# Kernel tuning notes

Hardware: AMD Instinct MI355X
Metric: run time of the kernel (lower is better)

Reference implementation:

```python
import jax, jax.numpy as jnp
import numpy as np

B, NQ, D, H, P, BEV, FFN = 8, 900, 256, 8, 4, 200, 512
HD = D // H
RADIUS = 0.2


def _ln(x, s, b):
    m = x.mean(-1, keepdims=True)
    v = ((x - m) ** 2).mean(-1, keepdims=True)
    return (x - m) / jnp.sqrt(v + 1e-5) * s + b


def _grid_sample(feat, grid):
    # feat: [BH, C, Hh, Ww]; grid: [BH, Q, P, 2] in [-1, 1]
    # bilinear, padding_mode='zeros', align_corners=False (matches F.grid_sample)
    BH, C, Hh, Ww = feat.shape
    gx = (grid[..., 0] + 1.0) * (Ww * 0.5) - 0.5
    gy = (grid[..., 1] + 1.0) * (Hh * 0.5) - 0.5
    x0 = jnp.floor(gx)
    y0 = jnp.floor(gy)
    wx1 = gx - x0
    wy1 = gy - y0

    def corner(xi, yi, w):
        valid = (xi >= 0) & (xi < Ww) & (yi >= 0) & (yi < Hh)
        xc = jnp.clip(xi, 0, Ww - 1).astype(jnp.int32)
        yc = jnp.clip(yi, 0, Hh - 1).astype(jnp.int32)
        vals = jax.vmap(lambda fm, yy, xx: fm[:, yy, xx])(feat, yc, xc)  # [BH, C, Q, P]
        return vals * (w * valid)[:, None, :, :]

    return (corner(x0, y0, (1 - wx1) * (1 - wy1))
            + corner(x0 + 1, y0, wx1 * (1 - wy1))
            + corner(x0, y0 + 1, (1 - wx1) * wy1)
            + corner(x0 + 1, y0 + 1, wx1 * wy1))


def _forward(query, memory, reference_points, query_pos,
             in_w, in_b, out_w, out_b,
             off_w, off_b, wt_w, wt_b, co_w, co_b,
             f_w1, f_b1, f_w2, f_b2,
             n1s, n1b, n2s, n2b, n3s, n3b, bev_h, bev_w):
    b, nq, d = query.shape
    # ---- self-attention (eval mode: dropout = identity) ----
    q_in = _ln(query + query_pos, n1s, n1b)
    qkv = q_in @ in_w.T + in_b
    q, k, v = jnp.split(qkv, 3, axis=-1)
    q = q.reshape(b, nq, H, HD)
    k = k.reshape(b, nq, H, HD)
    v = v.reshape(b, nq, H, HD)
    scores = jnp.einsum('bqhd,bkhd->bhqk', q, k) * (1.0 / HD ** 0.5)
    attn = jax.nn.softmax(scores, axis=-1)
    self_out = jnp.einsum('bhqk,bkhd->bqhd', attn, v).reshape(b, nq, d) @ out_w.T + out_b
    query = query + self_out
    # ---- deformable cross-attention over BEV memory ----
    q2 = _ln(query + query_pos, n2s, n2b)
    offsets = jnp.tanh(q2 @ off_w.T + off_b).reshape(b, nq, H, P, 2) * RADIUS
    weights = jax.nn.softmax((q2 @ wt_w.T + wt_b).reshape(b, nq, H, P), axis=-1)
    locations = reference_points[:, :, None, None, :2] + offsets  # [b, nq, H, P, 2]
    feat = memory.transpose(0, 2, 1).reshape(b * H, HD, bev_h, bev_w)
    grid = locations.transpose(0, 2, 1, 3, 4).reshape(b * H, nq, P, 2) * 2.0 - 1.0
    sampled = _grid_sample(feat, grid).reshape(b, H, HD, nq, P)
    fused = jnp.einsum('bhdqp,bqhp->bqhd', sampled, weights).reshape(b, nq, d)
    query = query + (fused @ co_w.T + co_b)
    # ---- FFN ----
    q3 = _ln(query, n3s, n3b)
    ffn = jax.nn.relu(q3 @ f_w1.T + f_b1) @ f_w2.T + f_b2
    return query + ffn


def setup_inputs() -> dict:
    key = jax.random.key(0)
    ks = jax.random.split(key, 16)
    s = 0.02
    return dict(
        query=jax.random.normal(ks[0], (B, NQ, D), jnp.float32),
        memory=jax.random.normal(ks[1], (B, BEV * BEV, D), jnp.float32),
        reference_points=jax.random.uniform(ks[2], (B, NQ, 2), jnp.float32),
        query_pos=jax.random.normal(ks[3], (B, NQ, D), jnp.float32),
        in_w=jax.random.normal(ks[4], (3 * D, D), jnp.float32) * s,
        in_b=jnp.zeros((3 * D,), jnp.float32),
        out_w=jax.random.normal(ks[5], (D, D), jnp.float32) * s,
        out_b=jnp.zeros((D,), jnp.float32),
        off_w=jax.random.normal(ks[6], (H * P * 2, D), jnp.float32) * s,
        off_b=jnp.zeros((H * P * 2,), jnp.float32),
        wt_w=jax.random.normal(ks[7], (H * P, D), jnp.float32) * s,
        wt_b=jnp.zeros((H * P,), jnp.float32),
        co_w=jax.random.normal(ks[8], (D, D), jnp.float32) * s,
        co_b=jnp.zeros((D,), jnp.float32),
        f_w1=jax.random.normal(ks[9], (FFN, D), jnp.float32) * s,
        f_b1=jnp.zeros((FFN,), jnp.float32),
        f_w2=jax.random.normal(ks[10], (D, FFN), jnp.float32) * s,
        f_b2=jnp.zeros((D,), jnp.float32),
        n1s=jnp.ones((D,), jnp.float32), n1b=jnp.zeros((D,), jnp.float32),
        n2s=jnp.ones((D,), jnp.float32), n2b=jnp.zeros((D,), jnp.float32),
        n3s=jnp.ones((D,), jnp.float32), n3b=jnp.zeros((D,), jnp.float32),
        bev_h=BEV, bev_w=BEV,
    )


def reference(query, memory, reference_points, query_pos,
              in_w, in_b, out_w, out_b,
              off_w, off_b, wt_w, wt_b, co_w, co_b,
              f_w1, f_b1, f_w2, f_b2,
              n1s, n1b, n2s, n2b, n3s, n3b, bev_h, bev_w):
    return _forward(query, memory, reference_points, query_pos,
                    in_w, in_b, out_w, out_b,
                    off_w, off_b, wt_w, wt_b, co_w, co_b,
                    f_w1, f_b1, f_w2, f_b2,
                    n1s, n1b, n2s, n2b, n3s, n3b, bev_h, bev_w)
```

## Files before the change

kernel.cpp:

```cpp
#include <hip/hip_runtime.h>
#include <math.h>

#define B_   8
#define NQ_  900
#define D_   256
#define H_   8
#define P_   4
#define BEV_ 200
#define FFN_ 512
#define HD_  32
#define M_   (B_*NQ_)
#define NKPAD 960

typedef __attribute__((ext_vector_type(8))) short short8;
typedef __attribute__((ext_vector_type(4))) float floatx4;

__device__ inline unsigned short f2bf(float f) {
    union { float f; unsigned u; } v; v.f = f;
    unsigned r = v.u + 0x7fffu + ((v.u >> 16) & 1u);
    return (unsigned short)(r >> 16);
}
__device__ inline float bf2f(unsigned short h) {
    union { unsigned u; float f; } v; v.u = ((unsigned)h) << 16;
    return v.f;
}

__global__ __launch_bounds__(256)
void convert_weights(const float* __restrict__ in_w, const float* __restrict__ out_w,
                     const float* __restrict__ off_w, const float* __restrict__ wt_w,
                     const float* __restrict__ co_w, const float* __restrict__ f_w1,
                     const float* __restrict__ f_w2, const float* __restrict__ off_b,
                     const float* __restrict__ wt_b,
                     unsigned short* __restrict__ wb, float* __restrict__ bias_ow)
{
    int i = blockIdx.x * 256 + threadIdx.x;
    if (i < 196608)      { wb[i] = f2bf(in_w[i]); }
    else if (i < 262144) { wb[i] = f2bf(out_w[i - 196608]); }
    else if (i < 278528) { wb[i] = f2bf(off_w[i - 262144]); }
    else if (i < 286720) { wb[i] = f2bf(wt_w[i - 278528]); }
    else if (i < 352256) { wb[i] = f2bf(co_w[i - 286720]); }
    else if (i < 483328) { wb[i] = f2bf(f_w1[i - 352256]); }
    else if (i < 614400) { wb[i] = f2bf(f_w2[i - 483328]); }
    else if (i < 614464) { bias_ow[i - 614400] = off_b[i - 614400]; }
    else if (i < 614496) { bias_ow[i - 614400] = wt_b[i - 614464]; }
}

__global__ __launch_bounds__(256)
void ln_kernel(const float* __restrict__ x, const float* __restrict__ pos,
               const float* __restrict__ gamma, const float* __restrict__ beta,
               unsigned short* __restrict__ out, int rows)
{
    int w    = threadIdx.x >> 6;
    int lane = threadIdx.x & 63;
    int row  = blockIdx.x * 4 + w;
    if (row >= rows) return;
    size_t base = (size_t)row * D_ + lane * 4;
    float4 v = *(const float4*)(x + base);
    if (pos) {
        float4 p = *(const float4*)(pos + base);
        v.x += p.x; v.y += p.y; v.z += p.z; v.w += p.w;
    }
    float s = v.x + v.y + v.z + v.w;
    float q = v.x*v.x + v.y*v.y + v.z*v.z + v.w*v.w;
    #pragma unroll
    for (int o = 1; o < 64; o <<= 1) {
        s += __shfl_xor(s, o, 64);
        q += __shfl_xor(q, o, 64);
    }
    float m   = s * (1.0f / D_);
    float var = q * (1.0f / D_) - m * m;
    float inv = rsqrtf(var + 1e-5f);
    float4 g = *(const float4*)(gamma + lane * 4);
    float4 b = *(const float4*)(beta  + lane * 4);
    ushort4 o4;
    o4.x = f2bf((v.x - m) * inv * g.x + b.x);
    o4.y = f2bf((v.y - m) * inv * g.y + b.y);
    o4.z = f2bf((v.z - m) * inv * g.z + b.z);
    o4.w = f2bf((v.w - m) * inv * g.w + b.w);
    *(ushort4*)(out + base) = o4;
}

template<int RELU, int OUTBF>
__global__ __launch_bounds__(256)
void gemm_mfma(const unsigned short* __restrict__ A, const unsigned short* __restrict__ W,
               const float* __restrict__ bias, const float* __restrict__ res,
               float* __restrict__ outf, unsigned short* __restrict__ outb,
               int M, int N, int K)
{
    __shared__ unsigned short As[128 * 32];
    __shared__ unsigned short Bs[128 * 32];
    const int t    = threadIdx.x;
    const int m0   = blockIdx.y * 128;
    const int n0   = blockIdx.x * 128;
    const int lane = t & 63;
    const int w    = t >> 6;
    const int wm   = (w >> 1) * 64;
    const int wn   = (w & 1) * 64;
    const int lr   = lane & 15;
    const int kq   = lane >> 4;

    floatx4 acc[4][4];
    #pragma unroll
    for (int i = 0; i < 4; ++i)
        #pragma unroll
        for (int j = 0; j < 4; ++j) acc[i][j] = (floatx4){0.f, 0.f, 0.f, 0.f};

    const int sr = t >> 1;
    const int sc = (t & 1) * 2;

    for (int k0 = 0; k0 < K; k0 += 32) {
        uint4 a0 = {0,0,0,0}, a1 = {0,0,0,0};
        int gm = m0 + sr;
        if (gm < M) {
            const uint4* src = (const uint4*)(A + (size_t)gm * K + k0 + sc * 8);
            a0 = src[0]; a1 = src[1];
        }
        *(uint4*)&As[sr * 32 + ((sc    ) ^ (sr & 3)) * 8] = a0;
        *(uint4*)&As[sr * 32 + ((sc + 1) ^ (sr & 3)) * 8] = a1;
        uint4 b0 = {0,0,0,0}, b1 = {0,0,0,0};
        int gn = n0 + sr;
        if (gn < N) {
            const uint4* src = (const uint4*)(W + (size_t)gn * K + k0 + sc * 8);
            b0 = src[0]; b1 = src[1];
        }
        *(uint4*)&Bs[sr * 32 + ((sc    ) ^ (sr & 3)) * 8] = b0;
        *(uint4*)&Bs[sr * 32 + ((sc + 1) ^ (sr & 3)) * 8] = b1;
        __syncthreads();

        short8 af[4], bfr[4];
        #pragma unroll
        for (int i = 0; i < 4; ++i) {
            int ra = wm + i * 16 + lr;
            af[i] = *(const short8*)&As[ra * 32 + (kq ^ (ra & 3)) * 8];
            int rb = wn + i * 16 + lr;
            bfr[i] = *(const short8*)&Bs[rb * 32 + (kq ^ (rb & 3)) * 8];
        }
        #pragma unroll
        for (int mi = 0; mi < 4; ++mi)
            #pragma unroll
            for (int ni = 0; ni < 4; ++ni)
                acc[mi][ni] = __builtin_amdgcn_mfma_f32_16x16x32_bf16(
                    af[mi], bfr[ni], acc[mi][ni], 0, 0, 0);
        __syncthreads();
    }

    const int rbase = kq * 4;
    #pragma unroll
    for (int ni = 0; ni < 4; ++ni) {
        int n = n0 + wn + ni * 16 + lr;
        if (n >= N) continue;
        float bv = bias[n];
        #pragma unroll
        for (int mi = 0; mi < 4; ++mi) {
            floatx4 c = acc[mi][ni];
            #pragma unroll
            for (int r = 0; r < 4; ++r) {
                int m = m0 + wm + mi * 16 + rbase + r;
                if (m < M) {
                    float vl = c[r] + bv;
                    if (res) vl += res[(size_t)m * N + n];
                    if (RELU) vl = fmaxf(vl, 0.f);
                    if (OUTBF) outb[(size_t)m * N + n] = f2bf(vl);
                    else       outf[(size_t)m * N + n] = vl;
                }
            }
        }
    }
}

__global__ __launch_bounds__(256)
void repack_qkv(const unsigned short* __restrict__ qkv,
                unsigned short* __restrict__ Qb, unsigned short* __restrict__ Kb,
                unsigned short* __restrict__ Vt)
{
    int tid = blockIdx.x * 256 + threadIdx.x;
    if (tid >= 64 * NKPAD * 32) return;
    int ch  = tid & 31;
    int key = (tid >> 5) % NKPAD;
    int bh  = tid / (NKPAD * 32);
    int b = bh >> 3, h = bh & 7;
    unsigned short qv = 0, kv = 0, vv = 0;
    if (key < NQ_) {
        const unsigned short* row = qkv + ((size_t)(b * NQ_ + key)) * 768 + h * 32 + ch;
        qv = f2bf(bf2f(row[0]) * 0.17677669529663687f);
        kv = row[256];
        vv = row[512];
    }
    size_t qk_idx = (size_t)bh * NKPAD * 32 + key * 32 + ch;
    Qb[qk_idx] = qv;
    Kb[qk_idx] = kv;
    Vt[(size_t)(bh * 32 + ch) * NKPAD + key] = vv;
}

__global__ __launch_bounds__(256)
void flash_attn(const unsigned short* __restrict__ Qb, const unsigned short* __restrict__ Kb,
                const unsigned short* __restrict__ Vt, unsigned short* __restrict__ out)
{
    __shared__ unsigned short P_lds[4][16][72];
    const int bh   = blockIdx.y;
    const int b    = bh >> 3, h = bh & 7;
    const int q0   = blockIdx.x * 64;
    const int w    = threadIdx.x >> 6;
    const int lane = threadIdx.x & 63;
    const int lr   = lane & 15;
    const int quad = lane >> 4;

    const short8 qfrag = *(const short8*)(Qb + ((size_t)bh * NKPAD + q0 + w * 16 + lr) * 32 + quad * 8);

    floatx4 O0 = (floatx4){0.f,0.f,0.f,0.f};
    floatx4 O1 = (floatx4){0.f,0.f,0.f,0.f};
    float m_i[4] = {-INFINITY, -INFINITY, -INFINITY, -INFINITY};
    float l_i[4] = {0.f, 0.f, 0.f, 0.f};

    const unsigned short* kbase_p = Kb + (size_t)bh * NKPAD * 32;
    const unsigned short* vbase_p = Vt + (size_t)bh * 32 * NKPAD;

    for (int kt = 0; kt < 15; ++kt) {
        const int kb = kt * 64;
        short8 kf[4];
        #pragma unroll
        for (int ni = 0; ni < 4; ++ni)
            kf[ni] = *(const short8*)(kbase_p + (size_t)(kb + ni * 16 + lr) * 32 + quad * 8);
        floatx4 S[4];
        #pragma unroll
        for (int ni = 0; ni < 4; ++ni)
            S[ni] = __builtin_amdgcn_mfma_f32_16x16x32_bf16(
                qfrag, kf[ni], (floatx4){0.f,0.f,0.f,0.f}, 0, 0, 0);
        if (kt == 14) {
            #pragma unroll
            for (int ni = 0; ni < 4; ++ni) {
                int key = kb + ni * 16 + lr;
                if (key >= NQ_) S[ni] = (floatx4){-1e30f, -1e30f, -1e30f, -1e30f};
            }
        }
        float rowmax[4];
        #pragma unroll
        for (int r = 0; r < 4; ++r)
            rowmax[r] = fmaxf(fmaxf(S[0][r], S[1][r]), fmaxf(S[2][r], S[3][r]));
        #pragma unroll
        for (int off = 1; off < 16; off <<= 1)
            #pragma unroll
            for (int r = 0; r < 4; ++r)
                rowmax[r] = fmaxf(rowmax[r], __shfl_xor(rowmax[r], off, 64));
        float alpha[4], rs[4];
        #pragma unroll
        for (int r = 0; r < 4; ++r) {
            float mnew = fmaxf(m_i[r], rowmax[r]);
            alpha[r] = __expf(m_i[r] - mnew);
            m_i[r] = mnew;
            rs[r] = 0.f;
        }
        #pragma unroll
        for (int ni = 0; ni < 4; ++ni) {
            #pragma unroll
            for (int r = 0; r < 4; ++r) {
                float p = __expf(S[ni][r] - m_i[r]);
                rs[r] += p;
                P_lds[w][quad * 4 + r][ni * 16 + lr] = f2bf(p);
            }
        }
        #pragma unroll
        for (int off = 1; off < 16; off <<= 1)
            #pragma unroll
            for (int r = 0; r < 4; ++r)
                rs[r] += __shfl_xor(rs[r], off, 64);
        #pragma unroll
        for (int r = 0; r < 4; ++r) {
            l_i[r] = alpha[r] * l_i[r] + rs[r];
            O0[r] *= alpha[r];
            O1[r] *= alpha[r];
        }
        asm volatile("s_waitcnt lgkmcnt(0)" ::: "memory");
        short8 pf0 = *(const short8*)&P_lds[w][lr][quad * 8];
        short8 pf1 = *(const short8*)&P_lds[w][lr][32 + quad * 8];
        short8 vf;
        vf = *(const short8*)(vbase_p + (size_t)(lr) * NKPAD + kb + quad * 8);
        O0 = __builtin_amdgcn_mfma_f32_16x16x32_bf16(pf0, vf, O0, 0, 0, 0);
        vf = *(const short8*)(vbase_p + (size_t)(lr) * NKPAD + kb + 32 + quad * 8);
        O0 = __builtin_amdgcn_mfma_f32_16x16x32_bf16(pf1, vf, O0, 0, 0, 0);
        vf = *(const short8*)(vbase_p + (size_t)(16 + lr) * NKPAD + kb + quad * 8);
        O1 = __builtin_amdgcn_mfma_f32_16x16x32_bf16(pf0, vf, O1, 0, 0, 0);
        vf = *(const short8*)(vbase_p + (size_t)(16 + lr) * NKPAD + kb + 32 + quad * 8);
        O1 = __builtin_amdgcn_mfma_f32_16x16x32_bf16(pf1, vf, O1, 0, 0, 0);
        asm volatile("s_waitcnt lgkmcnt(0)" ::: "memory");
    }
    #pragma unroll
    for (int r = 0; r < 4; ++r) {
        int q = q0 + w * 16 + quad * 4 + r;
        if (q < NQ_) {
            float inv = 1.f / l_i[r];
            size_t base = ((size_t)(b * NQ_ + q)) * D_ + h * 32;
            out[base + lr]      = f2bf(O0[r] * inv);
            out[base + 16 + lr] = f2bf(O1[r] * inv);
        }
    }
}

__global__ __launch_bounds__(256)
void prep_kernel(const float* __restrict__ offwt, const float* __restrict__ refp,
                 float4* __restrict__ sx, float4* __restrict__ sy, float4* __restrict__ sw)
{
    int idx = blockIdx.x * 256 + threadIdx.x;
    if (idx >= B_ * NQ_ * H_) return;
    int h  = idx & 7;
    int bq = idx >> 3;
    const float* orow = offwt + (size_t)bq * 96 + h * 8;
    const float* wrow = offwt + (size_t)bq * 96 + 64 + h * 4;
    float rx = refp[bq * 2 + 0];
    float ry = refp[bq * 2 + 1];
    float gx[4], gy[4], wv[4];
    #pragma unroll
    for (int p = 0; p < 4; ++p) {
        float ox = tanhf(orow[p * 2 + 0]) * 0.2f;
        float oy = tanhf(orow[p * 2 + 1]) * 0.2f;
        gx[p] = (rx + ox) * (float)BEV_ - 0.5f;
        gy[p] = (ry + oy) * (float)BEV_ - 0.5f;
        wv[p] = wrow[p];
    }
    float mx = fmaxf(fmaxf(wv[0], wv[1]), fmaxf(wv[2], wv[3]));
    float e0 = expf(wv[0]-mx), e1 = expf(wv[1]-mx), e2 = expf(wv[2]-mx), e3 = expf(wv[3]-mx);
    float inv = 1.f / (e0 + e1 + e2 + e3);
    sx[idx] = make_float4(gx[0], gx[1], gx[2], gx[3]);
    sy[idx] = make_float4(gy[0], gy[1], gy[2], gy[3]);
    sw[idx] = make_float4(e0*inv, e1*inv, e2*inv, e3*inv);
}

__global__ __launch_bounds__(256)
void sample_kernel(const float* __restrict__ mem,
                   const float4* __restrict__ sx, const float4* __restrict__ sy,
                   const float4* __restrict__ sw, unsigned short* __restrict__ fused)
{
    int tid = blockIdx.x * 256 + threadIdx.x;
    if (tid >= B_ * NQ_ * H_ * HD_) return;
    int d   = tid & 31;
    int bqh = tid >> 5;
    int h   = bqh & 7;
    int bq  = bqh >> 3;
    int b   = bq / NQ_;
    const float* mb = mem + (size_t)b * (BEV_ * BEV_) * D_ + h * HD_ + d;
    float4 X = sx[bqh], Y = sy[bqh], W = sw[bqh];
    float xs[4] = {X.x, X.y, X.z, X.w};
    float ys[4] = {Y.x, Y.y, Y.z, Y.w};
    float ws[4] = {W.x, W.y, W.z, W.w};
    float acc = 0.f;
    #pragma unroll
    for (int p = 0; p < 4; ++p) {
        float gx = xs[p], gy = ys[p];
        float x0f = floorf(gx), y0f = floorf(gy);
        int x0 = (int)x0f, y0 = (int)y0f;
        float wx1 = gx - x0f, wy1 = gy - y0f;
        float wx0 = 1.f - wx1, wy0 = 1.f - wy1;
        float s = 0.f;
        #pragma unroll
        for (int cy = 0; cy < 2; ++cy) {
            int yy = y0 + cy;
            if (yy < 0 || yy >= BEV_) continue;
            float wyv = cy ? wy1 : wy0;
            #pragma unroll
            for (int cx = 0; cx < 2; ++cx) {
                int xx = x0 + cx;
                if (xx < 0 || xx >= BEV_) continue;
                float wxv = cx ? wx1 : wx0;
                s += wyv * wxv * mb[((size_t)yy * BEV_ + xx) * D_];
            }
        }
        acc += ws[p] * s;
    }
    fused[(size_t)bq * D_ + h * HD_ + d] = f2bf(acc);
}

extern "C" void kernel_launch(void* const* d_in, const int* in_sizes, int n_in,
                              void* d_out, int out_size, void* d_ws, size_t ws_size,
                              hipStream_t stream) {
    const float* query     = (const float*)d_in[0];
    const float* memory    = (const float*)d_in[1];
    const float* refp      = (const float*)d_in[2];
    const float* query_pos = (const float*)d_in[3];
    const float* in_w  = (const float*)d_in[4];
    const float* in_b  = (const float*)d_in[5];
    const float* out_w = (const float*)d_in[6];
    const float* out_b = (const float*)d_in[7];
    const float* off_w = (const float*)d_in[8];
    const float* off_b = (const float*)d_in[9];
    const float* wt_w  = (const float*)d_in[10];
    const float* wt_b  = (const float*)d_in[11];
    const float* co_w  = (const float*)d_in[12];
    const float* co_b  = (const float*)d_in[13];
    const float* f_w1  = (const float*)d_in[14];
    const float* f_b1  = (const float*)d_in[15];
    const float* f_w2  = (const float*)d_in[16];
    const float* f_b2  = (const float*)d_in[17];
    const float* n1s = (const float*)d_in[18];
    const float* n1b = (const float*)d_in[19];
    const float* n2s = (const float*)d_in[20];
    const float* n2b = (const float*)d_in[21];
    const float* n3s = (const float*)d_in[22];
    const float* n3b = (const float*)d_in[23];
    float* outp = (float*)d_out;

    char* w = (char*)d_ws;
    unsigned short* wb      = (unsigned short*)w;
    float*          bias_ow = (float*)(w + 1228800);
    unsigned short* ln_bf   = (unsigned short*)(w + 1229184);
    float*          q1      = (float*)(w + 4915584);
    unsigned short* qkv_bf  = (unsigned short*)(w + 12288384);
    unsigned short* Qb      = (unsigned short*)(w + 23347584);
    unsigned short* Kb      = (unsigned short*)(w + 27279744);
    unsigned short* Vt      = (unsigned short*)(w + 31211904);
    float*          offwt   = (float*)(w + 12288384);
    float*          samp    = (float*)(w + 15053184);
    unsigned short* fuse_bf = (unsigned short*)(w + 17817984);
    unsigned short* h1_bf   = (unsigned short*)(w + 12288384);
    unsigned short* attn_bf = ln_bf;

    const unsigned short* wb_in  = wb;
    const unsigned short* wb_out = wb + 196608;
    const unsigned short* wb_ow  = wb + 262144;
    const unsigned short* wb_co  = wb + 286720;
    const unsigned short* wb_f1  = wb + 352256;
    const unsigned short* wb_f2  = wb + 483328;

    dim3 blk(256);
    const int M = M_;

    convert_weights<<<dim3((614496 + 255) / 256), blk, 0, stream>>>(
        in_w, out_w, off_w, wt_w, co_w, f_w1, f_w2, off_b, wt_b, wb, bias_ow);
    ln_kernel<<<dim3(M / 4), blk, 0, stream>>>(query, query_pos, n1s, n1b, ln_bf, M);
    gemm_mfma<0,1><<<dim3(6, 57), blk, 0, stream>>>(ln_bf, wb_in, in_b, nullptr,
                                                    nullptr, qkv_bf, M, 768, 256);
    repack_qkv<<<dim3(64 * NKPAD * 32 / 256), blk, 0, stream>>>(qkv_bf, Qb, Kb, Vt);
    flash_attn<<<dim3(15, 64), blk, 0, stream>>>(Qb, Kb, Vt, attn_bf);
    gemm_mfma<0,0><<<dim3(2, 57), blk, 0, stream>>>(attn_bf, wb_out, out_b, query,
                                                    q1, nullptr, M, 256, 256);
    ln_kernel<<<dim3(M / 4), blk, 0, stream>>>(q1, query_pos, n2s, n2b, ln_bf, M);
    gemm_mfma<0,0><<<dim3(1, 57), blk, 0, stream>>>(ln_bf, wb_ow, bias_ow, nullptr,
                                                    offwt, nullptr, M, 96, 256);
    prep_kernel<<<dim3((B_ * NQ_ * H_ + 255) / 256), blk, 0, stream>>>(
        offwt, refp, (float4*)samp, (float4*)samp + 57600, (float4*)samp + 115200);
    sample_kernel<<<dim3(B_ * NQ_ * H_ * HD_ / 256), blk, 0, stream>>>(
        memory, (const float4*)samp, (const float4*)samp + 57600,
        (const float4*)samp + 115200, fuse_bf);
    gemm_mfma<0,0><<<dim3(2, 57), blk, 0, stream>>>(fuse_bf, wb_co, co_b, q1,
                                                    outp, nullptr, M, 256, 256);
    ln_kernel<<<dim3(M / 4), blk, 0, stream>>>(outp, nullptr, n3s, n3b, ln_bf, M);
    gemm_mfma<1,1><<<dim3(4, 57), blk, 0, stream>>>(ln_bf, wb_f1, f_b1, nullptr,
                                                    nullptr, h1_bf, M, 512, 256);
    gemm_mfma<0,0><<<dim3(2, 57), blk, 0, stream>>>(h1_bf, wb_f2, f_b2, outp,
                                                    outp, nullptr, M, 256, 512);
}
```

Before: 680.6 us.

## Fuse QKV repack into GEMM epilogue, merge prologue kernels, fuse offset prep

The QKV projection GEMM now writes scaled Q, K and transposed V straight into the padded attention layouts, which removes the separate repack kernel and the intermediate qkv buffer. Weight conversion, zeroing of the padding rows and the first LayerNorm are merged into one prologue launch. The offset/weight GEMM stages its tile in LDS and computes the tanh offsets and softmax weights in its epilogue, replacing the prep kernel. Together these cut kernel launches and global round trips. The cost is scattered 2-byte stores in the QKV epilogue, plus extra LDS use in the fused offset GEMM.

```diff
diff --git a/kernel.cpp b/kernel.cpp
--- a/kernel.cpp
+++ b/kernel.cpp
@@ -26,23 +26,74 @@
 }
 
 __global__ __launch_bounds__(256)
-void convert_weights(const float* __restrict__ in_w, const float* __restrict__ out_w,
-                     const float* __restrict__ off_w, const float* __restrict__ wt_w,
-                     const float* __restrict__ co_w, const float* __restrict__ f_w1,
-                     const float* __restrict__ f_w2, const float* __restrict__ off_b,
-                     const float* __restrict__ wt_b,
-                     unsigned short* __restrict__ wb, float* __restrict__ bias_ow)
+void prologue(const float* __restrict__ in_w, const float* __restrict__ out_w,
+              const float* __restrict__ off_w, const float* __restrict__ wt_w,
+              const float* __restrict__ co_w, const float* __restrict__ f_w1,
+              const float* __restrict__ f_w2, const float* __restrict__ off_b,
+              const float* __restrict__ wt_b,
+              unsigned short* __restrict__ wb, float* __restrict__ bias_ow,
+              unsigned short* __restrict__ Qb, unsigned short* __restrict__ Kb,
+              unsigned short* __restrict__ Vt,
+              const float* __restrict__ query, const float* __restrict__ query_pos,
+              const float* __restrict__ n1s, const float* __restrict__ n1b,
+              unsigned short* __restrict__ ln_out)
 {
-    int i = blockIdx.x * 256 + threadIdx.x;
-    if (i < 196608)      { wb[i] = f2bf(in_w[i]); }
-    else if (i < 262144) { wb[i] = f2bf(out_w[i - 196608]); }
-    else if (i < 278528) { wb[i] = f2bf(off_w[i - 262144]); }
-    else if (i < 286720) { wb[i] = f2bf(wt_w[i - 278528]); }
-    else if (i < 352256) { wb[i] = f2bf(co_w[i - 286720]); }
-    else if (i < 483328) { wb[i] = f2bf(f_w1[i - 352256]); }
-    else if (i < 614400) { wb[i] = f2bf(f_w2[i - 483328]); }
-    else if (i < 614464) { bias_ow[i - 614400] = off_b[i - 614400]; }
-    else if (i < 614496) { bias_ow[i - 614400] = wt_b[i - 614464]; }
+    const int bx = blockIdx.x;
+    const int t  = threadIdx.x;
+    if (bx < 2401) {
+        int i = bx * 256 + t;
+        if (i < 196608)      { wb[i] = f2bf(in_w[i]); }
+        else if (i < 262144) { wb[i] = f2bf(out_w[i - 196608]); }
+        else if (i < 278528) { wb[i] = f2bf(off_w[i - 262144]); }
+        else if (i < 286720) { wb[i] = f2bf(wt_w[i - 278528]); }
+        else if (i < 352256) { wb[i] = f2bf(co_w[i - 286720]); }
+        else if (i < 483328) { wb[i] = f2bf(f_w1[i - 352256]); }
+        else if (i < 614400) { wb[i] = f2bf(f_w2[i - 483328]); }
+        else if (i < 614464) { bias_ow[i - 614400] = off_b[i - 614400]; }
+        else if (i < 614496) { bias_ow[i - 614400] = wt_b[i - 614464]; }
+    } else if (bx < 2881) {
+        int j  = (bx - 2401) * 256 + t;
+        int bh = j / 1920;
+        int rem = j - bh * 1920;
+        int q  = 900 + (rem >> 5);
+        int ch = rem & 31;
+        size_t idx = ((size_t)bh * NKPAD + q) * 32 + ch;
+        Qb[idx] = 0;
+        Kb[idx] = 0;
+    } else if (bx < 3361) {
+        int j  = (bx - 2881) * 256 + t;
+        int bh = j / 1920;
+        int rem = j - bh * 1920;
+        int ch = rem / 60;
+        int k  = rem - ch * 60;
+        Vt[((size_t)bh * 32 + ch) * NKPAD + 900 + k] = 0;
+    } else {
+        int w    = t >> 6;
+        int lane = t & 63;
+        int row  = (bx - 3361) * 4 + w;
+        size_t base = (size_t)row * D_ + lane * 4;
+        float4 v = *(const float4*)(query + base);
+        float4 p = *(const float4*)(query_pos + base);
+        v.x += p.x; v.y += p.y; v.z += p.z; v.w += p.w;
+        float s = v.x + v.y + v.z + v.w;
+        float q = v.x*v.x + v.y*v.y + v.z*v.z + v.w*v.w;
+        #pragma unroll
+        for (int o = 1; o < 64; o <<= 1) {
+            s += __shfl_xor(s, o, 64);
+            q += __shfl_xor(q, o, 64);
+        }
+        float m   = s * (1.0f / D_);
+        float var = q * (1.0f / D_) - m * m;
+        float inv = rsqrtf(var + 1e-5f);
+        float4 g = *(const float4*)(n1s + lane * 4);
+        float4 b = *(const float4*)(n1b + lane * 4);
+        ushort4 o4;
+        o4.x = f2bf((v.x - m) * inv * g.x + b.x);
+        o4.y = f2bf((v.y - m) * inv * g.y + b.y);
+        o4.z = f2bf((v.z - m) * inv * g.z + b.z);
+        o4.w = f2bf((v.w - m) * inv * g.w + b.w);
+        *(ushort4*)(ln_out + base) = o4;
+    }
 }
 
 __global__ __launch_bounds__(256)
@@ -80,11 +131,13 @@
     *(ushort4*)(out + base) = o4;
 }
 
-template<int RELU, int OUTBF>
+template<int RELU, int OUTBF, int QKVOUT>
 __global__ __launch_bounds__(256)
 void gemm_mfma(const unsigned short* __restrict__ A, const unsigned short* __restrict__ W,
                const float* __restrict__ bias, const float* __restrict__ res,
                float* __restrict__ outf, unsigned short* __restrict__ outb,
+               unsigned short* __restrict__ Qb, unsigned short* __restrict__ Kb,
+               unsigned short* __restrict__ Vt,
                int M, int N, int K)
 {
     __shared__ unsigned short As[128 * 32];
@@ -150,46 +203,157 @@
         int n = n0 + wn + ni * 16 + lr;
         if (n >= N) continue;
         float bv = bias[n];
+        if (QKVOUT) {
+            const int type = n >> 8;
+            const int hh   = (n >> 5) & 7;
+            const int ch   = n & 31;
+            #pragma unroll
+            for (int mi = 0; mi < 4; ++mi) {
+                floatx4 c = acc[mi][ni];
+                #pragma unroll
+                for (int r = 0; r < 4; ++r) {
+                    int m = m0 + wm + mi * 16 + rbase + r;
+                    if (m < M) {
+                        float vl = c[r] + bv;
+                        int bb = m / 900;
+                        int qq = m - bb * 900;
+                        size_t bh = (size_t)(bb * 8 + hh);
+                        if (type == 0)
+                            Qb[(bh * NKPAD + qq) * 32 + ch] = f2bf(vl * 0.17677669529663687f);
+                        else if (type == 1)
+                            Kb[(bh * NKPAD + qq) * 32 + ch] = f2bf(vl);
+                        else
+                            Vt[(bh * 32 + ch) * NKPAD + qq] = f2bf(vl);
+                    }
+                }
+            }
+        } else {
+            #pragma unroll
+            for (int mi = 0; mi < 4; ++mi) {
+                floatx4 c = acc[mi][ni];
+                #pragma unroll
+                for (int r = 0; r < 4; ++r) {
+                    int m = m0 + wm + mi * 16 + rbase + r;
+                    if (m < M) {
+                        float vl = c[r] + bv;
+                        if (res) vl += res[(size_t)m * N + n];
+                        if (RELU) vl = fmaxf(vl, 0.f);
+                        if (OUTBF) outb[(size_t)m * N + n] = f2bf(vl);
+                        else       outf[(size_t)m * N + n] = vl;
+                    }
+                }
+            }
+        }
+    }
+}
+
+__global__ __launch_bounds__(256)
+void gemm_offwt_prep(const unsigned short* __restrict__ A, const unsigned short* __restrict__ W,
+                     const float* __restrict__ bias, const float* __restrict__ refp,
+                     float4* __restrict__ sx, float4* __restrict__ sy, float4* __restrict__ sw)
+{
+    __shared__ unsigned short As[128 * 32];
+    __shared__ unsigned short Bs[128 * 32];
+    __shared__ float T[128][100];
+    const int t    = threadIdx.x;
+    const int m0   = blockIdx.y * 128;
+    const int lane = t & 63;
+    const int w    = t >> 6;
+    const int wm   = (w >> 1) * 64;
+    const int wn   = (w & 1) * 64;
+    const int lr   = lane & 15;
+    const int kq   = lane >> 4;
+    const int M = M_, N = 96, K = 256;
+
+    floatx4 acc[4][4];
+    #pragma unroll
+    for (int i = 0; i < 4; ++i)
+        #pragma unroll
+        for (int j = 0; j < 4; ++j) acc[i][j] = (floatx4){0.f, 0.f, 0.f, 0.f};
+
+    const int sr = t >> 1;
+    const int sc = (t & 1) * 2;
+
+    for (int k0 = 0; k0 < K; k0 += 32) {
+        uint4 a0 = {0,0,0,0}, a1 = {0,0,0,0};
+        int gm = m0 + sr;
+        if (gm < M) {
+            const uint4* src = (const uint4*)(A + (size_t)gm * K + k0 + sc * 8);
+            a0 = src[0]; a1 = src[1];
+        }
+        *(uint4*)&As[sr * 32 + ((sc    ) ^ (sr & 3)) * 8] = a0;
+        *(uint4*)&As[sr * 32 + ((sc + 1) ^ (sr & 3)) * 8] = a1;
+        uint4 b0 = {0,0,0,0}, b1 = {0,0,0,0};
+        int gn = sr;
+        if (gn < N) {
+            const uint4* src = (const uint4*)(W + (size_t)gn * K + k0 + sc * 8);
+            b0 = src[0]; b1 = src[1];
+        }
+        *(uint4*)&Bs[sr * 32 + ((sc    ) ^ (sr & 3)) * 8] = b0;
+        *(uint4*)&Bs[sr * 32 + ((sc + 1) ^ (sr & 3)) * 8] = b1;
+        __syncthreads();
+
+        short8 af[4], bfr[4];
+        #pragma unroll
+        for (int i = 0; i < 4; ++i) {
+            int ra = wm + i * 16 + lr;
+            af[i] = *(const short8*)&As[ra * 32 + (kq ^ (ra & 3)) * 8];
+            int rb = wn + i * 16 + lr;
+            bfr[i] = *(const short8*)&Bs[rb * 32 + (kq ^ (rb & 3)) * 8];
+        }
+        #pragma unroll
+        for (int mi = 0; mi < 4; ++mi)
+            #pragma unroll
+            for (int ni = 0; ni < 4; ++ni)
+                acc[mi][ni] = __builtin_amdgcn_mfma_f32_16x16x32_bf16(
+                    af[mi], bfr[ni], acc[mi][ni], 0, 0, 0);
+        __syncthreads();
+    }
+
+    const int rbase = kq * 4;
+    #pragma unroll
+    for (int ni = 0; ni < 4; ++ni) {
+        int n = wn + ni * 16 + lr;
+        if (n >= N) continue;
+        float bv = bias[n];
         #pragma unroll
         for (int mi = 0; mi < 4; ++mi) {
             floatx4 c = acc[mi][ni];
             #pragma unroll
-            for (int r = 0; r < 4; ++r) {
-                int m = m0 + wm + mi * 16 + rbase + r;
-                if (m < M) {
-                    float vl = c[r] + bv;
-                    if (res) vl += res[(size_t)m * N + n];
-                    if (RELU) vl = fmaxf(vl, 0.f);
-                    if (OUTBF) outb[(size_t)m * N + n] = f2bf(vl);
-                    else       outf[(size_t)m * N + n] = vl;
-                }
-            }
-        }
-    }
-}
-
-__global__ __launch_bounds__(256)
-void repack_qkv(const unsigned short* __restrict__ qkv,
-                unsigned short* __restrict__ Qb, unsigned short* __restrict__ Kb,
-                unsigned short* __restrict__ Vt)
-{
-    int tid = blockIdx.x * 256 + threadIdx.x;
-    if (tid >= 64 * NKPAD * 32) return;
-    int ch  = tid & 31;
-    int key = (tid >> 5) % NKPAD;
-    int bh  = tid / (NKPAD * 32);
-    int b = bh >> 3, h = bh & 7;
-    unsigned short qv = 0, kv = 0, vv = 0;
-    if (key < NQ_) {
-        const unsigned short* row = qkv + ((size_t)(b * NQ_ + key)) * 768 + h * 32 + ch;
-        qv = f2bf(bf2f(row[0]) * 0.17677669529663687f);
-        kv = row[256];
-        vv = row[512];
-    }
-    size_t qk_idx = (size_t)bh * NKPAD * 32 + key * 32 + ch;
-    Qb[qk_idx] = qv;
-    Kb[qk_idx] = kv;
-    Vt[(size_t)(bh * 32 + ch) * NKPAD + key] = vv;
+            for (int r = 0; r < 4; ++r)
+                T[wm + mi * 16 + rbase + r][n] = c[r] + bv;
+        }
+    }
+    __syncthreads();
+
+    #pragma unroll
+    for (int it = 0; it < 4; ++it) {
+        int item = t + it * 256;
+        int row  = item >> 3;
+        int h    = item & 7;
+        int gq   = m0 + row;
+        if (gq >= M) continue;
+        float rx = refp[gq * 2 + 0];
+        float ry = refp[gq * 2 + 1];
+        const float* orow = &T[row][h * 8];
+        const float* wrow = &T[row][64 + h * 4];
+        float gx[4], gy[4], wv[4];
+        #pragma unroll
+        for (int p = 0; p < 4; ++p) {
+            float ox = tanhf(orow[p * 2 + 0]) * 0.2f;
+            float oy = tanhf(orow[p * 2 + 1]) * 0.2f;
+            gx[p] = (rx + ox) * (float)BEV_ - 0.5f;
+            gy[p] = (ry + oy) * (float)BEV_ - 0.5f;
+            wv[p] = wrow[p];
+        }
+        float mx = fmaxf(fmaxf(wv[0], wv[1]), fmaxf(wv[2], wv[3]));
+        float e0 = expf(wv[0]-mx), e1 = expf(wv[1]-mx), e2 = expf(wv[2]-mx), e3 = expf(wv[3]-mx);
+        float inv = 1.f / (e0 + e1 + e2 + e3);
+        int idx = gq * 8 + h;
+        sx[idx] = make_float4(gx[0], gx[1], gx[2], gx[3]);
+        sy[idx] = make_float4(gy[0], gy[1], gy[2], gy[3]);
+        sw[idx] = make_float4(e0*inv, e1*inv, e2*inv, e3*inv);
+    }
 }
 
 __global__ __launch_bounds__(256)
@@ -294,35 +458,6 @@
             out[base + 16 + lr] = f2bf(O1[r] * inv);
         }
     }
-}
-
-__global__ __launch_bounds__(256)
-void prep_kernel(const float* __restrict__ offwt, const float* __restrict__ refp,
-                 float4* __restrict__ sx, float4* __restrict__ sy, float4* __restrict__ sw)
-{
-    int idx = blockIdx.x * 256 + threadIdx.x;
-    if (idx >= B_ * NQ_ * H_) return;
-    int h  = idx & 7;
-    int bq = idx >> 3;
-    const float* orow = offwt + (size_t)bq * 96 + h * 8;
-    const float* wrow = offwt + (size_t)bq * 96 + 64 + h * 4;
-    float rx = refp[bq * 2 + 0];
-    float ry = refp[bq * 2 + 1];
-    float gx[4], gy[4], wv[4];
-    #pragma unroll
-    for (int p = 0; p < 4; ++p) {
-        float ox = tanhf(orow[p * 2 + 0]) * 0.2f;
-        float oy = tanhf(orow[p * 2 + 1]) * 0.2f;
-        gx[p] = (rx + ox) * (float)BEV_ - 0.5f;
-        gy[p] = (ry + oy) * (float)BEV_ - 0.5f;
-        wv[p] = wrow[p];
-    }
-    float mx = fmaxf(fmaxf(wv[0], wv[1]), fmaxf(wv[2], wv[3]));
-    float e0 = expf(wv[0]-mx), e1 = expf(wv[1]-mx), e2 = expf(wv[2]-mx), e3 = expf(wv[3]-mx);
-    float inv = 1.f / (e0 + e1 + e2 + e3);
-    sx[idx] = make_float4(gx[0], gx[1], gx[2], gx[3]);
-    sy[idx] = make_float4(gy[0], gy[1], gy[2], gy[3]);
-    sw[idx] = make_float4(e0*inv, e1*inv, e2*inv, e3*inv);
 }
 
 __global__ __launch_bounds__(256)
@@ -403,11 +538,9 @@
     float*          bias_ow = (float*)(w + 1228800);
     unsigned short* ln_bf   = (unsigned short*)(w + 1229184);
     float*          q1      = (float*)(w + 4915584);
-    unsigned short* qkv_bf  = (unsigned short*)(w + 12288384);
     unsigned short* Qb      = (unsigned short*)(w + 23347584);
     unsigned short* Kb      = (unsigned short*)(w + 27279744);
     unsigned short* Vt      = (unsigned short*)(w + 31211904);
-    float*          offwt   = (float*)(w + 12288384);
     float*          samp    = (float*)(w + 15053184);
     unsigned short* fuse_bf = (unsigned short*)(w + 17817984);
     unsigned short* h1_bf   = (unsigned short*)(w + 12288384);
@@ -423,28 +556,31 @@
     dim3 blk(256);
     const int M = M_;
 
-    convert_weights<<<dim3((614496 + 255) / 256), blk, 0, stream>>>(
-        in_w, out_w, off_w, wt_w, co_w, f_w1, f_w2, off_b, wt_b, wb, bias_ow);
-    ln_kernel<<<dim3(M / 4), blk, 0, stream>>>(query, query_pos, n1s, n1b, ln_bf, M);
-    gemm_mfma<0,1><<<dim3(6, 57), blk, 0, stream>>>(ln_bf, wb_in, in_b, nullptr,
-                                                    nullptr, qkv_bf, M, 768, 256);
-    repack_qkv<<<dim3(64 * NKPAD * 32 / 256), blk, 0, stream>>>(qkv_bf, Qb, Kb, Vt);
+    prologue<<<dim3(5161), blk, 0, stream>>>(
+        in_w, out_w, off_w, wt_w, co_w, f_w1, f_w2, off_b, wt_b, wb, bias_ow,
+        Qb, Kb, Vt, query, query_pos, n1s, n1b, ln_bf);
+    gemm_mfma<0,0,1><<<dim3(6, 57), blk, 0, stream>>>(ln_bf, wb_in, in_b, nullptr,
+                                                      nullptr, nullptr, Qb, Kb, Vt,
+                                                      M, 768, 256);
     flash_attn<<<dim3(15, 64), blk, 0, stream>>>(Qb, Kb, Vt, attn_bf);
-    gemm_mfma<0,0><<<dim3(2, 57), blk, 0, stream>>>(attn_bf, wb_out, out_b, query,
-                                                    q1, nullptr, M, 256, 256);
+    gemm_mfma<0,0,0><<<dim3(2, 57), blk, 0, stream>>>(attn_bf, wb_out, out_b, query,
+                                                      q1, nullptr, nullptr, nullptr, nullptr,
+                                                      M, 256, 256);
     ln_kernel<<<dim3(M / 4), blk, 0, stream>>>(q1, query_pos, n2s, n2b, ln_bf, M);
-    gemm_mfma<0,0><<<dim3(1, 57), blk, 0, stream>>>(ln_bf, wb_ow, bias_ow, nullptr,
-                                                    offwt, nullptr, M, 96, 256);
-    prep_kernel<<<dim3((B_ * NQ_ * H_ + 255) / 256), blk, 0, stream>>>(
-        offwt, refp, (float4*)samp, (float4*)samp + 57600, (float4*)samp + 115200);
+    gemm_offwt_prep<<<dim3(1, 57), blk, 0, stream>>>(
+        ln_bf, wb_ow, bias_ow, refp,
+        (float4*)samp, (float4*)samp + 57600, (float4*)samp + 115200);
     sample_kernel<<<dim3(B_ * NQ_ * H_ * HD_ / 256), blk, 0, stream>>>(
         memory, (const float4*)samp, (const float4*)samp + 57600,
         (const float4*)samp + 115200, fuse_bf);
-    gemm_mfma<0,0><<<dim3(2, 57), blk, 0, stream>>>(fuse_bf, wb_co, co_b, q1,
-                                                    outp, nullptr, M, 256, 256);
+    gemm_mfma<0,0,0><<<dim3(2, 57), blk, 0, stream>>>(fuse_bf, wb_co, co_b, q1,
+                                                      outp, nullptr, nullptr, nullptr, nullptr,
+                                                      M, 256, 256);
     ln_kernel<<<dim3(M / 4), blk, 0, stream>>>(outp, nullptr, n3s, n3b, ln_bf, M);
-    gemm_mfma<1,1><<<dim3(4, 57), blk, 0, stream>>>(ln_bf, wb_f1, f_b1, nullptr,
-                                                    nullptr, h1_bf, M, 512, 256);
-    gemm_mfma<0,0><<<dim3(2, 57), blk, 0, stream>>>(h1_bf, wb_f2, f_b2, outp,
-                                                    outp, nullptr, M, 256, 512);
-}
+    gemm_mfma<1,1,0><<<dim3(4, 57), blk, 0, stream>>>(ln_bf, wb_f1, f_b1, nullptr,
+                                                      nullptr, h1_bf, nullptr, nullptr, nullptr,
+                                                      M, 512, 256);
+    gemm_mfma<0,0,0><<<dim3(2, 57), blk, 0, stream>>>(h1_bf, wb_f2, f_b2, outp,
+                                                      outp, nullptr, nullptr, nullptr, nullptr,
+                                                      M, 256, 512);
+}
```

Result: faster. 663.7 us (-2.5%).
